# Kernel optimization log

Measured on AMD Instinct MI355X. Metric: run time of the kernel, lower is better.

The kernel has to match this reference:

```python
import jax, jax.numpy as jnp
import numpy as np

N = 100000   # nodes
E = 3200000  # edges
IN = 5
H = 128
L = 6
EPS = 1e-5

def _bn(x, g, b):
    # BatchNorm1d in training mode: batch stats over node dim, biased variance
    m = jnp.mean(x, axis=0)
    v = jnp.mean((x - m) ** 2, axis=0)
    return (x - m) * jax.lax.rsqrt(v + EPS) * g + b

def setup_inputs() -> dict:
    key = jax.random.key(0)
    ks = jax.random.split(key, 20)
    x = jax.random.normal(ks[0], (N, IN), dtype=jnp.float32)
    edge_index = jax.random.randint(ks[1], (2, E), 0, N, dtype=jnp.int64)
    batch = jnp.zeros((N,), dtype=jnp.int64)
    s = 0.05
    return {
        "x": x, "edge_index": edge_index, "batch": batch,
        "in_W": jax.random.normal(ks[2], (IN, H), jnp.float32) * s,
        "in_b": jnp.zeros((H,), jnp.float32),
        "in_g": jnp.ones((H,), jnp.float32),
        "in_beta": jnp.zeros((H,), jnp.float32),
        "conv_W": jax.random.normal(ks[3], (L, H, H), jnp.float32) * s,
        "conv_b": jnp.zeros((L, H), jnp.float32),
        "bn_g": jnp.ones((L, H), jnp.float32),
        "bn_beta": jnp.zeros((L, H), jnp.float32),
        "pW1": jax.random.normal(ks[4], (H, 32), jnp.float32) * s,
        "pb1": jnp.zeros((32,), jnp.float32),
        "pW2": jax.random.normal(ks[5], (32, 1), jnp.float32) * s,
        "pb2": jnp.zeros((1,), jnp.float32),
        "vW1": jax.random.normal(ks[6], (H, 64), jnp.float32) * s,
        "vb1": jnp.zeros((64,), jnp.float32),
        "vW2": jax.random.normal(ks[7], (64, 1), jnp.float32) * s,
        "vb2": jnp.zeros((1,), jnp.float32),
    }

def reference(x, edge_index, batch, in_W, in_b, in_g, in_beta,
              conv_W, conv_b, bn_g, bn_beta,
              pW1, pb1, pW2, pb2, vW1, vb1, vW2, vb2):
    n = x.shape[0]
    # GCN normalization with self-loops (computed once; depends only on edge_index)
    loops = jnp.arange(n, dtype=edge_index.dtype)
    src = jnp.concatenate([edge_index[0], loops])
    dst = jnp.concatenate([edge_index[1], loops])
    deg = jax.ops.segment_sum(jnp.ones_like(dst, dtype=x.dtype), dst, num_segments=n)
    dinv = jnp.where(deg > 0, jax.lax.rsqrt(deg), 0.0)
    norm = dinv[src] * dinv[dst]  # [E+N]

    def gcn(h, W, b):
        h = h @ W
        msg = h[src] * norm[:, None]
        return jax.ops.segment_sum(msg, dst, num_segments=n) + b

    h = jax.nn.relu(_bn(x @ in_W + in_b, in_g, in_beta))
    for i in range(L):
        h = jax.nn.relu(_bn(gcn(h, conv_W[i], conv_b[i]), bn_g[i], bn_beta[i])) + h

    policy_logits = (jax.nn.relu(h @ pW1 + pb1) @ pW2 + pb2)[:, 0]  # [N]

    # global_mean_pool over batch ids (single graph here, num_segments=1)
    num_graphs = 1
    sums = jax.ops.segment_sum(h, batch, num_segments=num_graphs)
    cnts = jax.ops.segment_sum(jnp.ones((n,), h.dtype), batch, num_segments=num_graphs)
    g = sums / jnp.maximum(cnts, 1.0)[:, None]  # [1, H]
    value = jnp.tanh(jax.nn.relu(g @ vW1 + vb1) @ vW2 + vb2)[:, 0]  # [1]
    return policy_logits, value
```

## Files before the change

### kernel.cpp

```cpp
#include <hip/hip_runtime.h>
#include <hip/hip_bf16.h>

typedef __hip_bfloat16 bf16;
typedef long long i64;
typedef unsigned short u16;
typedef __attribute__((ext_vector_type(8))) short bf16x8;
typedef __attribute__((ext_vector_type(4))) float f32x4;

#define EPSV 1e-5f
#define WINLEN 2560
#define CHUNK 64

static __device__ __forceinline__ float ldf(const void* p, size_t i, int fb) {
  return fb ? __bfloat162float(((const bf16*)p)[i]) : ((const float*)p)[i];
}
static __device__ __forceinline__ u16 f2b(float f) {
  unsigned int u = __float_as_uint(f);
  u += 0x7FFF + ((u >> 16) & 1);
  return (u16)(u >> 16);
}
static __device__ __forceinline__ float rb2f(u16 u) {
  return __uint_as_float(((unsigned int)u) << 16);
}
static __device__ __forceinline__ unsigned pk2(float a, float b) {
  return (unsigned)f2b(a) | ((unsigned)f2b(b) << 16);
}
static __device__ __forceinline__ float lo2f(unsigned w) { return __uint_as_float(w << 16); }
static __device__ __forceinline__ float hi2f(unsigned w) { return __uint_as_float(w & 0xFFFF0000u); }


__global__ void setup_kernel(const int* __restrict__ ei_w, const unsigned int* __restrict__ g,
                             int* __restrict__ eflag, int* __restrict__ fflag,
                             int* __restrict__ degcnt, int* __restrict__ fill,
                             int* __restrict__ wctr, int n) {
  int i = blockIdx.x * 256 + threadIdx.x;
  if (i < n) { degcnt[i] = 0; fill[i] = 0; }
  if (blockIdx.x == 0) {
    __shared__ int nz;
    if (threadIdx.x == 0) nz = 0;
    if (threadIdx.x < 32) wctr[threadIdx.x] = 0;
    __syncthreads();
    for (int k = threadIdx.x; k < 1024; k += 256)
      if (ei_w[2 * k + 1] != 0) atomicAdd(&nz, 1);
    __syncthreads();
    if (threadIdx.x == 0) {
      *eflag = (nz == 0) ? 1 : 0;
      *fflag = (g[0] == 0x3F803F80u) ? 1 : 0;
    }
  }
}


__global__ void __launch_bounds__(256) pre_merged_kernel(
    const void* __restrict__ x, const void* __restrict__ W, const void* __restrict__ b,
    const void* __restrict__ ei, const void* __restrict__ convW,
    const int* __restrict__ eflag, const int* __restrict__ fflag,
    int* __restrict__ degcnt, u16* __restrict__ pre, float* __restrict__ pi,
    u16* __restrict__ wf, int n, int in_dim, int e, int wtotal, int gi, int gf) {
  __shared__ float4 SS[256], QQ[256];
  int fb = *fflag;
  if ((int)blockIdx.x < gi) {
    int q = threadIdx.x & 31, g8 = threadIdx.x >> 5;
    int c = q * 4;
    float b0 = ldf(b, c, fb), b1 = ldf(b, c + 1, fb), b2v = ldf(b, c + 2, fb), b3 = ldf(b, c + 3, fb);
    float s0 = 0, s1 = 0, s2 = 0, s3 = 0, q0 = 0, q1 = 0, q2 = 0, q3 = 0;
    for (int node = blockIdx.x * 8 + g8; node < n; node += gi * 8) {
      float a0 = b0, a1 = b1, a2 = b2v, a3 = b3;
      for (int k = 0; k < in_dim; ++k) {
        float xv = ldf(x, (size_t)node * in_dim + k, fb);
        size_t w0 = (size_t)k * 128 + c;
        a0 = fmaf(xv, ldf(W, w0, fb), a0);
        a1 = fmaf(xv, ldf(W, w0 + 1, fb), a1);
        a2 = fmaf(xv, ldf(W, w0 + 2, fb), a2);
        a3 = fmaf(xv, ldf(W, w0 + 3, fb), a3);
      }
      unsigned w0p = pk2(a0, a1), w1p = pk2(a2, a3);
      *(uint2*)(pre + (size_t)node * 128 + c) = make_uint2(w0p, w1p);
      float r0 = lo2f(w0p), r1 = hi2f(w0p), r2 = lo2f(w1p), r3 = hi2f(w1p);
      s0 += r0; s1 += r1; s2 += r2; s3 += r3;
      q0 = fmaf(r0, r0, q0); q1 = fmaf(r1, r1, q1); q2 = fmaf(r2, r2, q2); q3 = fmaf(r3, r3, q3);
    }
    SS[threadIdx.x] = make_float4(s0, s1, s2, s3);
    QQ[threadIdx.x] = make_float4(q0, q1, q2, q3);
    __syncthreads();
    if (threadIdx.x < 32) {
      float4 a = SS[threadIdx.x], qq = QQ[threadIdx.x];
      for (int g = 1; g < 8; ++g) {
        float4 u = SS[g * 32 + threadIdx.x], w = QQ[g * 32 + threadIdx.x];
        a.x += u.x; a.y += u.y; a.z += u.z; a.w += u.w;
        qq.x += w.x; qq.y += w.y; qq.z += w.z; qq.w += w.w;
      }
      int cc = threadIdx.x * 4;
      *(float4*)(pi + (size_t)blockIdx.x * 256 + cc) = a;
      *(float4*)(pi + (size_t)blockIdx.x * 256 + 128 + cc) = qq;
    }
  } else if ((int)blockIdx.x < gi + gf) {
    int bid = blockIdx.x - gi;
    int k = bid & 7;
    int lo = (int)(((long long)n * k) >> 3);
    int hi = (int)(((long long)n * (k + 1)) >> 3);
    int stride = (gf >> 3) * 256;
    int fb64 = *eflag;
    for (int i = (bid >> 3) * 256 + threadIdx.x; i < e; i += stride) {
      int d;
      if (fb64) d = (int)((const i64*)ei)[(size_t)e + i];
      else      d = ((const int*)ei)[(size_t)e + i];
      if (d >= lo && d < hi) atomicAdd(&degcnt[d], 1);
    }
  } else {
    int bid = blockIdx.x - gi - gf;
    int i = bid * 256 + threadIdx.x;
    if (i < wtotal) {
      int l = i >> 14, r = i & 16383;
      int k = r >> 7, nn = r & 127;
      int s = k >> 5, quad = (k >> 3) & 3, j = k & 7;
      int ct = nn >> 4, n16 = nn & 15;
      wf[(size_t)l * 16384 + (ct * 4 + s) * 512 + quad * 128 + n16 * 8 + j] = f2b(ldf(convW, i, fb));
    }
  }
}


__global__ void __launch_bounds__(256) scanA_kernel(const int* __restrict__ deg,
                                                    int* __restrict__ rp,
                                                    int* __restrict__ bsum,
                                                    float* __restrict__ dinv, int n) {
  int base = blockIdx.x * 1024 + threadIdx.x * 4;
  int v0 = (base     < n) ? deg[base]     : 0;
  int v1 = (base + 1 < n) ? deg[base + 1] : 0;
  int v2 = (base + 2 < n) ? deg[base + 2] : 0;
  int v3 = (base + 3 < n) ? deg[base + 3] : 0;
  if (base     < n) dinv[base]     = rsqrtf((float)v0 + 1.0f);
  if (base + 1 < n) dinv[base + 1] = rsqrtf((float)v1 + 1.0f);
  if (base + 2 < n) dinv[base + 2] = rsqrtf((float)v2 + 1.0f);
  if (base + 3 < n) dinv[base + 3] = rsqrtf((float)v3 + 1.0f);
  int ts = v0 + v1 + v2 + v3;
  __shared__ int ls[256];
  ls[threadIdx.x] = ts;
  __syncthreads();
  for (int off = 1; off < 256; off <<= 1) {
    int u = (threadIdx.x >= off) ? ls[threadIdx.x - off] : 0;
    __syncthreads();
    ls[threadIdx.x] += u;
    __syncthreads();
  }
  int run = ls[threadIdx.x] - ts;
  if (base     < n) rp[base]     = run; run += v0;
  if (base + 1 < n) rp[base + 1] = run; run += v1;
  if (base + 2 < n) rp[base + 2] = run; run += v2;
  if (base + 3 < n) rp[base + 3] = run;
  if (threadIdx.x == 255) bsum[blockIdx.x] = ls[255];
}

__global__ void __launch_bounds__(256) scanB_kernel(int* __restrict__ bsum, int* __restrict__ rp,
                                                    int nb, int n, int e) {
  __shared__ int ls[256];
  int t = threadIdx.x;
  int v = (t < nb) ? bsum[t] : 0;
  ls[t] = v;
  __syncthreads();
  for (int off = 1; off < 256; off <<= 1) {
    int u = (t >= off) ? ls[t - off] : 0;
    __syncthreads();
    ls[t] += u;
    __syncthreads();
  }
  if (t < nb) bsum[t] = ls[t] - v;
  if (t == 0) rp[n] = e;
}

__global__ void scanC_kernel(int* __restrict__ rp, const int* __restrict__ bsum, int n) {
  int i = blockIdx.x * 256 + threadIdx.x;
  if (i < n) rp[i] += bsum[i >> 10];
}

__global__ void fill_kernel(const void* __restrict__ ei, const int* __restrict__ flag,
                            const int* __restrict__ row_ptr,
                            int* __restrict__ fill, int* __restrict__ csr_src, int e, int n) {
  int k = blockIdx.x & 7;
  int lo = (int)(((long long)n * k) >> 3);
  int hi = (int)(((long long)n * (k + 1)) >> 3);
  int stride = (gridDim.x >> 3) * 256;
  int fb64 = *flag;
  for (int i = (blockIdx.x >> 3) * 256 + threadIdx.x; i < e; i += stride) {
    int d;
    if (fb64) d = (int)((const i64*)ei)[(size_t)e + i];
    else      d = ((const int*)ei)[(size_t)e + i];
    if (d < lo || d >= hi) continue;
    int s;
    if (fb64) s = (int)((const i64*)ei)[i];
    else      s = ((const int*)ei)[i];
    int pos = row_ptr[d] + atomicAdd(&fill[d], 1);
    csr_src[pos] = s;
  }
}

__global__ void __launch_bounds__(1024) finalize_inproj_kernel(
    const float* __restrict__ pi, int nb,
    const void* __restrict__ g, const void* __restrict__ beta,
    const int* __restrict__ fflag,
    float* __restrict__ scale, float* __restrict__ shift,
    float inv_n) {
  __shared__ float RS[8][128], RQ[8][128];
  int fb = *fflag;
  int c = threadIdx.x & 127, r = threadIdx.x >> 7;
  float s = 0.f, s2 = 0.f;
#pragma unroll 4
  for (int b = r; b < nb; b += 8) {
    s  += pi[(size_t)b * 256 + c];
    s2 += pi[(size_t)b * 256 + 128 + c];
  }
  RS[r][c] = s; RQ[r][c] = s2;
  __syncthreads();
  if (threadIdx.x < 128) {
    float ts = 0.f, tq = 0.f;
#pragma unroll
    for (int i = 0; i < 8; ++i) { ts += RS[i][c]; tq += RQ[i][c]; }
    float mean = ts * inv_n;
    float var = tq * inv_n - mean * mean;
    float sc = ldf(g, c, fb) * rsqrtf(var + EPSV);
    scale[c] = sc;
    shift[c] = ldf(beta, c, fb) - mean * sc;
  }
}


__global__ void __launch_bounds__(256) gemm_bn_kernel(
    const u16* __restrict__ pre, u16* __restrict__ hbuf,
    const float* __restrict__ scale, const float* __restrict__ shift,
    const u16* __restrict__ wfL, const float* __restrict__ dinv,
    u16* __restrict__ u, int n, int use_res) {
  __shared__ u16 At[4][2048];
  int lane = threadIdx.x & 63;
  int wave = threadIdx.x >> 6;
  int n16 = lane & 15, quad = lane >> 4;
  u16* at = At[wave];
  int node = lane & 15;
  int cgrp = lane >> 4;
  int ntiles = (n + 15) >> 4;
  for (int tile = blockIdx.x * 4 + wave; tile < ntiles; tile += gridDim.x * 4) {
    int n0 = tile * 16;
    int gn = n0 + node;
#pragma unroll
    for (int r = 0; r < 8; ++r) {
      int c4 = r * 4 + cgrp;
      int c = c4 * 4;
      float4 h4 = make_float4(0.f, 0.f, 0.f, 0.f);
      if (gn < n) {
        uint2 pv = *(const uint2*)(pre + (size_t)gn * 128 + c);
        float4 sc = *(const float4*)(scale + c);
        float4 sh = *(const float4*)(shift + c);
        h4.x = fmaxf(fmaf(lo2f(pv.x), sc.x, sh.x), 0.f);
        h4.y = fmaxf(fmaf(hi2f(pv.x), sc.y, sh.y), 0.f);
        h4.z = fmaxf(fmaf(lo2f(pv.y), sc.z, sh.z), 0.f);
        h4.w = fmaxf(fmaf(hi2f(pv.y), sc.w, sh.w), 0.f);
        if (use_res) {
          uint2 rv = *(const uint2*)(hbuf + (size_t)gn * 128 + c);
          h4.x += lo2f(rv.x); h4.y += hi2f(rv.x);
          h4.z += lo2f(rv.y); h4.w += hi2f(rv.y);
        }
        *(uint2*)(hbuf + (size_t)gn * 128 + c) = make_uint2(pk2(h4.x, h4.y), pk2(h4.z, h4.w));
      }
      ushort4 uu;
      uu.x = f2b(h4.x); uu.y = f2b(h4.y); uu.z = f2b(h4.z); uu.w = f2b(h4.w);
      int s = c4 >> 3, qd = (c4 >> 1) & 3, j0 = (c4 & 1) * 4;
      *(ushort4*)(at + s * 512 + qd * 128 + node * 8 + j0) = uu;
    }
    __builtin_amdgcn_s_waitcnt(0);
    f32x4 acc[8];
#pragma unroll
    for (int ct = 0; ct < 8; ++ct) acc[ct] = (f32x4){0.f, 0.f, 0.f, 0.f};
#pragma unroll
    for (int s = 0; s < 4; ++s) {
      bf16x8 af = *(const bf16x8*)(at + s * 512 + lane * 8);
#pragma unroll
      for (int ct = 0; ct < 8; ++ct) {
        bf16x8 bfr = *(const bf16x8*)(wfL + (size_t)(ct * 4 + s) * 512 + lane * 8);
        acc[ct] = __builtin_amdgcn_mfma_f32_16x16x32_bf16(af, bfr, acc[ct], 0, 0, 0);
      }
    }
    float dv[4];
#pragma unroll
    for (int r = 0; r < 4; ++r) {
      int row = n0 + quad * 4 + r;
      dv[r] = (row < n) ? dinv[row] : 0.f;
    }
#pragma unroll
    for (int ct = 0; ct < 8; ++ct) {
#pragma unroll
      for (int r = 0; r < 4; ++r) {
        int row = n0 + quad * 4 + r;
        if (row < n)
          u[((size_t)(ct >> 1) * n + row) * 32 + (ct & 1) * 16 + n16] = f2b(acc[ct][r] * dv[r]);
      }
    }
  }
}


__global__ void __launch_bounds__(256) gather_stats_kernel(
    const int* __restrict__ row_ptr, const int* __restrict__ csr_src,
    const u16* __restrict__ u, const float* __restrict__ dinv,
    const void* __restrict__ b, const int* __restrict__ fflag,
    u16* __restrict__ pre, float* __restrict__ pg,
    int* __restrict__ wctr, int n, int nch, size_t bOff) {
  __shared__ int sm[WINLEN];
  __shared__ float SW[4][4][8], QW[4][4][8];
  __shared__ int curchunk;
  int fb = *fflag;
  int ct2 = blockIdx.x & 3;
  const u16* us = u + (size_t)ct2 * n * 32;
  int q = threadIdx.x & 3;
  int g = threadIdx.x >> 2;
  int c = ct2 * 32 + q * 8;
  float bias[8];
#pragma unroll
  for (int i = 0; i < 8; ++i) bias[i] = ldf(b, bOff + c + i, fb);
  float sA[8], qA[8];
#pragma unroll
  for (int i = 0; i < 8; ++i) { sA[i] = 0.f; qA[i] = 0.f; }

  for (;;) {
    __syncthreads();
    if (threadIdx.x == 0) curchunk = atomicAdd(&wctr[ct2], 1);
    __syncthreads();
    int ch = curchunk;
    if (ch >= nch) break;
    int c0 = ch * CHUNK;
    int node = c0 + g;
    int valid = node < n;
    int beg = valid ? row_ptr[node] : 0;
    int end = valid ? row_ptr[node + 1] : 0;
    int cend = c0 + CHUNK; if (cend > n) cend = n;
    int chunk_lo = row_ptr[c0];
    int chunk_hi = row_ptr[cend];
    float acc[8];
    if (valid) {
      uint4 su = *(const uint4*)(us + (size_t)node * 32 + q * 8);
      acc[0] = lo2f(su.x); acc[1] = hi2f(su.x);
      acc[2] = lo2f(su.y); acc[3] = hi2f(su.y);
      acc[4] = lo2f(su.z); acc[5] = hi2f(su.z);
      acc[6] = lo2f(su.w); acc[7] = hi2f(su.w);
    } else {
#pragma unroll
      for (int i = 0; i < 8; ++i) acc[i] = 0.f;
    }
    for (int wlo = chunk_lo; wlo < chunk_hi; wlo += WINLEN) {
      int wlen = chunk_hi - wlo; if (wlen > WINLEN) wlen = WINLEN;
      __syncthreads();
      for (int i = threadIdx.x; i < wlen; i += 256)
        sm[i] = __builtin_nontemporal_load(csr_src + wlo + i);
      __syncthreads();
      int j0 = beg > wlo ? beg : wlo;
      int j1 = end < wlo + wlen ? end : wlo + wlen;
      int j = j0;
#define ACC(UU) \
      acc[0] += lo2f(UU.x); acc[1] += hi2f(UU.x); \
      acc[2] += lo2f(UU.y); acc[3] += hi2f(UU.y); \
      acc[4] += lo2f(UU.z); acc[5] += hi2f(UU.z); \
      acc[6] += lo2f(UU.w); acc[7] += hi2f(UU.w);
      for (; j + 8 <= j1; j += 8) {
        int i0 = sm[j - wlo],     i1 = sm[j - wlo + 1], i2 = sm[j - wlo + 2], i3 = sm[j - wlo + 3];
        int i4 = sm[j - wlo + 4], i5 = sm[j - wlo + 5], i6 = sm[j - wlo + 6], i7 = sm[j - wlo + 7];
        uint4 U0 = *(const uint4*)(us + (size_t)i0 * 32 + q * 8);
        uint4 U1 = *(const uint4*)(us + (size_t)i1 * 32 + q * 8);
        uint4 U2 = *(const uint4*)(us + (size_t)i2 * 32 + q * 8);
        uint4 U3 = *(const uint4*)(us + (size_t)i3 * 32 + q * 8);
        uint4 U4 = *(const uint4*)(us + (size_t)i4 * 32 + q * 8);
        uint4 U5 = *(const uint4*)(us + (size_t)i5 * 32 + q * 8);
        uint4 U6 = *(const uint4*)(us + (size_t)i6 * 32 + q * 8);
        uint4 U7 = *(const uint4*)(us + (size_t)i7 * 32 + q * 8);
        ACC(U0) ACC(U1) ACC(U2) ACC(U3) ACC(U4) ACC(U5) ACC(U6) ACC(U7)
      }
      for (; j + 4 <= j1; j += 4) {
        int i0 = sm[j - wlo], i1 = sm[j - wlo + 1], i2 = sm[j - wlo + 2], i3 = sm[j - wlo + 3];
        uint4 U0 = *(const uint4*)(us + (size_t)i0 * 32 + q * 8);
        uint4 U1 = *(const uint4*)(us + (size_t)i1 * 32 + q * 8);
        uint4 U2 = *(const uint4*)(us + (size_t)i2 * 32 + q * 8);
        uint4 U3 = *(const uint4*)(us + (size_t)i3 * 32 + q * 8);
        ACC(U0) ACC(U1) ACC(U2) ACC(U3)
      }
      for (; j < j1; ++j) {
        int i0 = sm[j - wlo];
        uint4 U0 = *(const uint4*)(us + (size_t)i0 * 32 + q * 8);
        ACC(U0)
      }
#undef ACC
    }
    if (valid) {
      float dv = dinv[node];
      float o0 = fmaf(acc[0], dv, bias[0]), o1 = fmaf(acc[1], dv, bias[1]);
      float o2 = fmaf(acc[2], dv, bias[2]), o3 = fmaf(acc[3], dv, bias[3]);
      float o4 = fmaf(acc[4], dv, bias[4]), o5 = fmaf(acc[5], dv, bias[5]);
      float o6 = fmaf(acc[6], dv, bias[6]), o7 = fmaf(acc[7], dv, bias[7]);
      unsigned w0 = pk2(o0, o1), w1 = pk2(o2, o3), w2 = pk2(o4, o5), w3 = pk2(o6, o7);
      *(uint4*)(pre + (size_t)node * 128 + c) = make_uint4(w0, w1, w2, w3);
      float r0 = lo2f(w0), r1 = hi2f(w0), r2 = lo2f(w1), r3 = hi2f(w1);
      float r4 = lo2f(w2), r5 = hi2f(w2), r6 = lo2f(w3), r7 = hi2f(w3);
      sA[0] += r0; sA[1] += r1; sA[2] += r2; sA[3] += r3;
      sA[4] += r4; sA[5] += r5; sA[6] += r6; sA[7] += r7;
      qA[0] = fmaf(r0, r0, qA[0]); qA[1] = fmaf(r1, r1, qA[1]);
      qA[2] = fmaf(r2, r2, qA[2]); qA[3] = fmaf(r3, r3, qA[3]);
      qA[4] = fmaf(r4, r4, qA[4]); qA[5] = fmaf(r5, r5, qA[5]);
      qA[6] = fmaf(r6, r6, qA[6]); qA[7] = fmaf(r7, r7, qA[7]);
    }
  }
#pragma unroll
  for (int m = 4; m <= 32; m <<= 1) {
#pragma unroll
    for (int i = 0; i < 8; ++i) {
      sA[i] += __shfl_xor(sA[i], m, 64);
      qA[i] += __shfl_xor(qA[i], m, 64);
    }
  }
  int lane = threadIdx.x & 63, wv = threadIdx.x >> 6;
  if (lane < 4) {
#pragma unroll
    for (int i = 0; i < 8; ++i) { SW[wv][lane][i] = sA[i]; QW[wv][lane][i] = qA[i]; }
  }
  __syncthreads();
  if (threadIdx.x < 32) {
    int qq = threadIdx.x >> 3, i = threadIdx.x & 7;
    float a = SW[0][qq][i] + SW[1][qq][i] + SW[2][qq][i] + SW[3][qq][i];
    float b2 = QW[0][qq][i] + QW[1][qq][i] + QW[2][qq][i] + QW[3][qq][i];
    pg[(size_t)blockIdx.x * 64 + qq * 8 + i] = a;
    pg[(size_t)blockIdx.x * 64 + 32 + qq * 8 + i] = b2;
  }
}

__global__ void __launch_bounds__(1024) finalize_gather_kernel(
    const float* __restrict__ pg, int nbG,
    const void* __restrict__ g, const void* __restrict__ beta,
    const int* __restrict__ fflag,
    float* __restrict__ scale, float* __restrict__ shift,
    float inv_n, size_t off) {
  __shared__ float RS[8][128], RQ[8][128];
  int fb = *fflag;
  int c = threadIdx.x & 127, r = threadIdx.x >> 7;
  int ct2 = c >> 5, ic = c & 31;
  float s = 0.f, s2 = 0.f;
#pragma unroll 4
  for (int b = ct2 + 4 * r; b < nbG; b += 32) {
    s  += pg[(size_t)b * 64 + ic];
    s2 += pg[(size_t)b * 64 + 32 + ic];
  }
  RS[r][c] = s; RQ[r][c] = s2;
  __syncthreads();
  if (threadIdx.x < 128) {
    float ts = 0.f, tq = 0.f;
#pragma unroll
    for (int i = 0; i < 8; ++i) { ts += RS[i][c]; tq += RQ[i][c]; }
    float mean = ts * inv_n;
    float var = tq * inv_n - mean * mean;
    float sc = ldf(g, off + c, fb) * rsqrtf(var + EPSV);
    scale[c] = sc;
    shift[c] = ldf(beta, off + c, fb) - mean * sc;
  }
}


__global__ void __launch_bounds__(256) policy_pool_kernel(
    const u16* __restrict__ pre, const u16* __restrict__ hbuf,
    const float* __restrict__ scale, const float* __restrict__ shift,
    const void* __restrict__ pW1, const void* __restrict__ pb1,
    const void* __restrict__ pW2, const void* __restrict__ pb2,
    const int* __restrict__ fflag, float* __restrict__ pp,
    void* __restrict__ out, int n) {
  __shared__ float W1[128 * 32];
  __shared__ float B1v[32], W2v[32];
  int fb = *fflag;
  for (int i = threadIdx.x; i < 128 * 32; i += 256) W1[i] = ldf(pW1, i, fb);
  if (threadIdx.x < 32) {
    B1v[threadIdx.x] = ldf(pb1, threadIdx.x, fb);
    W2v[threadIdx.x] = ldf(pW2, threadIdx.x, fb);
  }
  __syncthreads();
  float bias2 = ldf(pb2, 0, fb);
  int q = threadIdx.x & 31, g8 = threadIdx.x >> 5;
  int c = q * 4;
  float4 sc = *(const float4*)(scale + c);
  float4 sh = *(const float4*)(shift + c);
  float cs0 = 0, cs1 = 0, cs2 = 0, cs3 = 0;
  for (int node = blockIdx.x * 8 + g8; node < n; node += gridDim.x * 8) {
    uint2 pv = *(const uint2*)(pre + (size_t)node * 128 + c);
    uint2 rv = *(const uint2*)(hbuf + (size_t)node * 128 + c);
    float4 h4;
    h4.x = fmaxf(fmaf(lo2f(pv.x), sc.x, sh.x), 0.f) + lo2f(rv.x);
    h4.y = fmaxf(fmaf(hi2f(pv.x), sc.y, sh.y), 0.f) + hi2f(rv.x);
    h4.z = fmaxf(fmaf(lo2f(pv.y), sc.z, sh.z), 0.f) + lo2f(rv.y);
    h4.w = fmaxf(fmaf(hi2f(pv.y), sc.w, sh.w), 0.f) + hi2f(rv.y);
    cs0 += h4.x; cs1 += h4.y; cs2 += h4.z; cs3 += h4.w;
    float acc = B1v[q];
#pragma unroll
    for (int k4 = 0; k4 < 32; ++k4) {
      float hx = __shfl(h4.x, k4, 32);
      float hy = __shfl(h4.y, k4, 32);
      float hz = __shfl(h4.z, k4, 32);
      float hw = __shfl(h4.w, k4, 32);
      int k = k4 * 4;
      acc = fmaf(hx, W1[k * 32 + q], acc);
      acc = fmaf(hy, W1[(k + 1) * 32 + q], acc);
      acc = fmaf(hz, W1[(k + 2) * 32 + q], acc);
      acc = fmaf(hw, W1[(k + 3) * 32 + q], acc);
    }
    acc = fmaxf(acc, 0.f) * W2v[q];
    for (int off = 16; off; off >>= 1) acc += __shfl_down(acc, off, 32);
    if (q == 0) {
      float v = acc + bias2;
      if (fb) ((bf16*)out)[node] = __float2bfloat16(v);
      else    ((float*)out)[node] = v;
    }
  }
  __shared__ float4 SS[256];
  SS[threadIdx.x] = make_float4(cs0, cs1, cs2, cs3);
  __syncthreads();
  if (threadIdx.x < 32) {
    float4 a = SS[threadIdx.x];
    for (int g = 1; g < 8; ++g) {
      float4 u = SS[g * 32 + threadIdx.x];
      a.x += u.x; a.y += u.y; a.z += u.z; a.w += u.w;
    }
    *(float4*)(pp + (size_t)blockIdx.x * 128 + threadIdx.x * 4) = a;
  }
}

__global__ void __launch_bounds__(1024) value_kernel(
    const float* __restrict__ pp, int nbP,
    const void* __restrict__ vW1, const void* __restrict__ vb1,
    const void* __restrict__ vW2, const void* __restrict__ vb2,
    const int* __restrict__ fflag,
    void* __restrict__ out, int n, float inv_n) {
  __shared__ float RS[8][128];
  __shared__ float gs[128];
  int fb = *fflag;
  int c = threadIdx.x & 127, r = threadIdx.x >> 7;
  float s = 0.f;
#pragma unroll 4
  for (int b = r; b < nbP; b += 8) s += pp[(size_t)b * 128 + c];
  RS[r][c] = s;
  __syncthreads();
  if (threadIdx.x < 128) {
    float t = 0.f;
#pragma unroll
    for (int i = 0; i < 8; ++i) t += RS[i][c];
    gs[c] = t;
  }
  __syncthreads();
  if (threadIdx.x < 64) {
    int cc = threadIdx.x;
    float acc = ldf(vb1, cc, fb);
    for (int k = 0; k < 128; ++k) acc = fmaf(gs[k] * inv_n, ldf(vW1, (size_t)k * 64 + cc, fb), acc);
    acc = fmaxf(acc, 0.f);
    float v = acc * ldf(vW2, cc, fb);
    for (int off = 32; off; off >>= 1) v += __shfl_down(v, off, 64);
    if (cc == 0) {
      float rr = tanhf(v + ldf(vb2, 0, fb));
      if (fb) ((bf16*)out)[n] = __float2bfloat16(rr);
      else    ((float*)out)[n] = rr;
    }
  }
}


extern "C" void kernel_launch(void* const* d_in, const int* in_sizes, int n_in,
                              void* d_out, int out_size, void* d_ws, size_t ws_size,
                              hipStream_t stream) {
  const void* x       = d_in[0];
  const void* ei      = d_in[1];
  const void* in_W    = d_in[3];
  const void* in_b    = d_in[4];
  const void* in_g    = d_in[5];
  const void* in_beta = d_in[6];
  const void* conv_W  = d_in[7];
  const void* conv_b  = d_in[8];
  const void* bn_g    = d_in[9];
  const void* bn_beta = d_in[10];
  const void* pW1     = d_in[11];
  const void* pb1     = d_in[12];
  const void* pW2     = d_in[13];
  const void* pb2     = d_in[14];
  const void* vW1     = d_in[15];
  const void* vb1     = d_in[16];
  const void* vW2     = d_in[17];
  const void* vb2     = d_in[18];

  const int H = 128;
  int in_dim = in_sizes[3] / H;
  int n      = in_sizes[0] / in_dim;
  int e      = in_sizes[1] / 2;
  int L      = in_sizes[7] / (H * H);

  const int GS  = 2048;
  const int GI  = 512;
  const int GP  = 1024;
  const int GF  = 2048;

  char* w = (char*)d_ws;
  u16*   u    = (u16*)w;   w += (size_t)n * H * sizeof(u16);
  u16*   pre  = (u16*)w;   w += (size_t)n * H * sizeof(u16);
  u16*   hbuf = (u16*)w;   w += (size_t)n * H * sizeof(u16);
  int*   csr_src  = (int*)w;   w += ((size_t)e + 16) * sizeof(int);
  int*   row_ptr  = (int*)w;   w += (size_t)(n + 1 + 15) / 16 * 16 * sizeof(int);
  int*   degcnt   = (int*)w;   w += (size_t)n * sizeof(int);
  int*   fillc    = (int*)w;   w += (size_t)n * sizeof(int);
  float* dinv     = (float*)w; w += (size_t)n * sizeof(float);
  float* scale = (float*)w; w += 128 * sizeof(float);
  float* shift = (float*)w; w += 128 * sizeof(float);
  int*   eflag = (int*)w;   w += 16 * sizeof(int);
  int*   fflag = (int*)w;   w += 16 * sizeof(int);
  int*   bsum  = (int*)w;   w += 256 * sizeof(int);
  int*   wctr  = (int*)w;   w += 32 * sizeof(int);
  u16*   wf    = (u16*)w;   w += (size_t)L * H * H * sizeof(u16);
  float* pi    = (float*)w; w += (size_t)GI * 256 * sizeof(float);
  float* pg    = (float*)w; w += (size_t)GS * 64 * sizeof(float);
  float* pp    = (float*)w; w += (size_t)GP * 128 * sizeof(float);

  int gN = (n + 255) / 256;
  int nb = (n + 1023) >> 10;
  int nch = (n + CHUNK - 1) / CHUNK;
  int wtotal = L * H * H;
  int GW = (wtotal + 255) / 256;
  float inv_n = 1.0f / (float)n;

  setup_kernel<<<gN, 256, 0, stream>>>((const int*)ei, (const unsigned int*)in_g,
                                       eflag, fflag, degcnt, fillc, wctr, n);
  pre_merged_kernel<<<GI + GF + GW, 256, 0, stream>>>(
      x, in_W, in_b, ei, conv_W, eflag, fflag, degcnt, pre, pi, wf,
      n, in_dim, e, wtotal, GI, GF);
  scanA_kernel<<<nb, 256, 0, stream>>>(degcnt, row_ptr, bsum, dinv, n);
  scanB_kernel<<<1, 256, 0, stream>>>(bsum, row_ptr, nb, n, e);
  scanC_kernel<<<gN, 256, 0, stream>>>(row_ptr, bsum, n);
  fill_kernel<<<GF, 256, 0, stream>>>(ei, eflag, row_ptr, fillc, csr_src, e, n);
  finalize_inproj_kernel<<<1, 1024, 0, stream>>>(pi, GI, in_g, in_beta, fflag, scale, shift, inv_n);

  for (int l = 0; l < L; ++l) {
    gemm_bn_kernel<<<2048, 256, 0, stream>>>(pre, hbuf, scale, shift, wf + (size_t)l * H * H,
                                             dinv, u, n, (l > 0) ? 1 : 0);
    gather_stats_kernel<<<GS, 256, 0, stream>>>(row_ptr, csr_src, u, dinv,
                                                conv_b, fflag, pre, pg, wctr + l * 4,
                                                n, nch, (size_t)l * H);
    finalize_gather_kernel<<<1, 1024, 0, stream>>>(pg, GS, bn_g, bn_beta, fflag, scale, shift,
                                                   inv_n, (size_t)l * H);
  }

  policy_pool_kernel<<<GP, 256, 0, stream>>>(pre, hbuf, scale, shift, pW1, pb1, pW2, pb2,
                                             fflag, pp, d_out, n);
  value_kernel<<<1, 1024, 0, stream>>>(pp, GP, vW1, vb1, vW2, vb2, fflag, d_out, n, inv_n);
}
```

Baseline: 1.721 ms.

## Partition CSR by source-node bucket so gathers stay within a cache-sized source range

Builds a bucketed CSR: edges are counted and placed per (source bucket, destination) slot, with 8 buckets chosen by shifting the source id. The scan now runs over 8n entries with a multi-pass block-sum scan, and the degree/dinv computation moves into scanC by summing the per-bucket counts. The gather kernel loops over buckets so that at any moment the blocks read u rows from one source range, which is meant to improve L2/MALL locality of the random row reads. In exchange it adds 8x more row-pointer reads and scan work, more window loop overhead per chunk, and larger count arrays.

```diff
diff --git a/kernel.cpp b/kernel.cpp
--- a/kernel.cpp
+++ b/kernel.cpp
@@ -10,6 +10,7 @@
 #define EPSV 1e-5f
 #define WINLEN 2560
 #define CHUNK 64
+#define NBUK 8
 
 static __device__ __forceinline__ float ldf(const void* p, size_t i, int fb) {
   return fb ? __bfloat162float(((const bf16*)p)[i]) : ((const float*)p)[i];
@@ -31,10 +32,10 @@
 
 __global__ void setup_kernel(const int* __restrict__ ei_w, const unsigned int* __restrict__ g,
                              int* __restrict__ eflag, int* __restrict__ fflag,
-                             int* __restrict__ degcnt, int* __restrict__ fill,
-                             int* __restrict__ wctr, int n) {
+                             int* __restrict__ deg2, int* __restrict__ fill2,
+                             int* __restrict__ wctr, int m8) {
   int i = blockIdx.x * 256 + threadIdx.x;
-  if (i < n) { degcnt[i] = 0; fill[i] = 0; }
+  if (i < m8) { deg2[i] = 0; fill2[i] = 0; }
   if (blockIdx.x == 0) {
     __shared__ int nz;
     if (threadIdx.x == 0) nz = 0;
@@ -55,8 +56,8 @@
     const void* __restrict__ x, const void* __restrict__ W, const void* __restrict__ b,
     const void* __restrict__ ei, const void* __restrict__ convW,
     const int* __restrict__ eflag, const int* __restrict__ fflag,
-    int* __restrict__ degcnt, u16* __restrict__ pre, float* __restrict__ pi,
-    u16* __restrict__ wf, int n, int in_dim, int e, int wtotal, int gi, int gf) {
+    int* __restrict__ deg2, u16* __restrict__ pre, float* __restrict__ pi,
+    u16* __restrict__ wf, int n, int in_dim, int e, int wtotal, int gi, int gf, int shift) {
   __shared__ float4 SS[256], QQ[256];
   int fb = *fflag;
   if ((int)blockIdx.x < gi) {
@@ -105,7 +106,13 @@
       int d;
       if (fb64) d = (int)((const i64*)ei)[(size_t)e + i];
       else      d = ((const int*)ei)[(size_t)e + i];
-      if (d >= lo && d < hi) atomicAdd(&degcnt[d], 1);
+      if (d >= lo && d < hi) {
+        int s;
+        if (fb64) s = (int)((const i64*)ei)[i];
+        else      s = ((const int*)ei)[i];
+        int bk = s >> shift;
+        atomicAdd(&deg2[(size_t)bk * n + d], 1);
+      }
     }
   } else {
     int bid = blockIdx.x - gi - gf;
@@ -123,17 +130,12 @@
 
 __global__ void __launch_bounds__(256) scanA_kernel(const int* __restrict__ deg,
                                                     int* __restrict__ rp,
-                                                    int* __restrict__ bsum,
-                                                    float* __restrict__ dinv, int n) {
+                                                    int* __restrict__ bsum, int m) {
   int base = blockIdx.x * 1024 + threadIdx.x * 4;
-  int v0 = (base     < n) ? deg[base]     : 0;
-  int v1 = (base + 1 < n) ? deg[base + 1] : 0;
-  int v2 = (base + 2 < n) ? deg[base + 2] : 0;
-  int v3 = (base + 3 < n) ? deg[base + 3] : 0;
-  if (base     < n) dinv[base]     = rsqrtf((float)v0 + 1.0f);
-  if (base + 1 < n) dinv[base + 1] = rsqrtf((float)v1 + 1.0f);
-  if (base + 2 < n) dinv[base + 2] = rsqrtf((float)v2 + 1.0f);
-  if (base + 3 < n) dinv[base + 3] = rsqrtf((float)v3 + 1.0f);
+  int v0 = (base     < m) ? deg[base]     : 0;
+  int v1 = (base + 1 < m) ? deg[base + 1] : 0;
+  int v2 = (base + 2 < m) ? deg[base + 2] : 0;
+  int v3 = (base + 3 < m) ? deg[base + 3] : 0;
   int ts = v0 + v1 + v2 + v3;
   __shared__ int ls[256];
   ls[threadIdx.x] = ts;
@@ -145,38 +147,57 @@
     __syncthreads();
   }
   int run = ls[threadIdx.x] - ts;
-  if (base     < n) rp[base]     = run; run += v0;
-  if (base + 1 < n) rp[base + 1] = run; run += v1;
-  if (base + 2 < n) rp[base + 2] = run; run += v2;
-  if (base + 3 < n) rp[base + 3] = run;
+  if (base     < m) rp[base]     = run; run += v0;
+  if (base + 1 < m) rp[base + 1] = run; run += v1;
+  if (base + 2 < m) rp[base + 2] = run; run += v2;
+  if (base + 3 < m) rp[base + 3] = run;
   if (threadIdx.x == 255) bsum[blockIdx.x] = ls[255];
 }
 
 __global__ void __launch_bounds__(256) scanB_kernel(int* __restrict__ bsum, int* __restrict__ rp,
-                                                    int nb, int n, int e) {
+                                                    int nb, int m, int e) {
   __shared__ int ls[256];
+  __shared__ int carry;
   int t = threadIdx.x;
-  int v = (t < nb) ? bsum[t] : 0;
-  ls[t] = v;
-  __syncthreads();
-  for (int off = 1; off < 256; off <<= 1) {
-    int u = (t >= off) ? ls[t - off] : 0;
-    __syncthreads();
-    ls[t] += u;
-    __syncthreads();
-  }
-  if (t < nb) bsum[t] = ls[t] - v;
-  if (t == 0) rp[n] = e;
-}
-
-__global__ void scanC_kernel(int* __restrict__ rp, const int* __restrict__ bsum, int n) {
+  if (t == 0) carry = 0;
+  __syncthreads();
+  for (int base = 0; base < nb; base += 256) {
+    int v = (base + t < nb) ? bsum[base + t] : 0;
+    ls[t] = v;
+    __syncthreads();
+    for (int off = 1; off < 256; off <<= 1) {
+      int u = (t >= off) ? ls[t - off] : 0;
+      __syncthreads();
+      ls[t] += u;
+      __syncthreads();
+    }
+    int ex = ls[t] - v + carry;
+    if (base + t < nb) bsum[base + t] = ex;
+    int tot = ls[255];
+    __syncthreads();
+    if (t == 0) carry += tot;
+    __syncthreads();
+  }
+  if (t == 0) rp[m] = e;
+}
+
+__global__ void scanC_kernel(int* __restrict__ rp, const int* __restrict__ bsum,
+                             const int* __restrict__ deg2, float* __restrict__ dinv,
+                             int n, int m) {
   int i = blockIdx.x * 256 + threadIdx.x;
-  if (i < n) rp[i] += bsum[i >> 10];
+  if (i < m) rp[i] += bsum[i >> 10];
+  if (i < n) {
+    int t = 0;
+#pragma unroll
+    for (int b = 0; b < NBUK; ++b) t += deg2[(size_t)b * n + i];
+    dinv[i] = rsqrtf((float)t + 1.0f);
+  }
 }
 
 __global__ void fill_kernel(const void* __restrict__ ei, const int* __restrict__ flag,
-                            const int* __restrict__ row_ptr,
-                            int* __restrict__ fill, int* __restrict__ csr_src, int e, int n) {
+                            const int* __restrict__ rp2,
+                            int* __restrict__ fill2, int* __restrict__ csr_src,
+                            int e, int n, int shift) {
   int k = blockIdx.x & 7;
   int lo = (int)(((long long)n * k) >> 3);
   int hi = (int)(((long long)n * (k + 1)) >> 3);
@@ -190,8 +211,10 @@
     int s;
     if (fb64) s = (int)((const i64*)ei)[i];
     else      s = ((const int*)ei)[i];
-    int pos = row_ptr[d] + atomicAdd(&fill[d], 1);
-    csr_src[pos] = s;
+    int bk = s >> shift;
+    size_t slot = (size_t)bk * n + d;
+    int pos = rp2[slot] + atomicAdd(&fill2[slot], 1);
+    __builtin_nontemporal_store(s, &csr_src[pos]);
   }
 }
 
@@ -299,7 +322,7 @@
 
 
 __global__ void __launch_bounds__(256) gather_stats_kernel(
-    const int* __restrict__ row_ptr, const int* __restrict__ csr_src,
+    const int* __restrict__ rp2, const int* __restrict__ csr_src,
     const u16* __restrict__ u, const float* __restrict__ dinv,
     const void* __restrict__ b, const int* __restrict__ fflag,
     u16* __restrict__ pre, float* __restrict__ pg,
@@ -329,11 +352,7 @@
     int c0 = ch * CHUNK;
     int node = c0 + g;
     int valid = node < n;
-    int beg = valid ? row_ptr[node] : 0;
-    int end = valid ? row_ptr[node + 1] : 0;
     int cend = c0 + CHUNK; if (cend > n) cend = n;
-    int chunk_lo = row_ptr[c0];
-    int chunk_hi = row_ptr[cend];
     float acc[8];
     if (valid) {
       uint4 su = *(const uint4*)(us + (size_t)node * 32 + q * 8);
@@ -345,47 +364,54 @@
 #pragma unroll
       for (int i = 0; i < 8; ++i) acc[i] = 0.f;
     }
-    for (int wlo = chunk_lo; wlo < chunk_hi; wlo += WINLEN) {
-      int wlen = chunk_hi - wlo; if (wlen > WINLEN) wlen = WINLEN;
-      __syncthreads();
-      for (int i = threadIdx.x; i < wlen; i += 256)
-        sm[i] = __builtin_nontemporal_load(csr_src + wlo + i);
-      __syncthreads();
-      int j0 = beg > wlo ? beg : wlo;
-      int j1 = end < wlo + wlen ? end : wlo + wlen;
-      int j = j0;
+    for (int bk = 0; bk < NBUK; ++bk) {
+      const int* rpb = rp2 + (size_t)bk * n;
+      int beg = valid ? rpb[node] : 0;
+      int end = valid ? rpb[node + 1] : 0;
+      int chunk_lo = rpb[c0];
+      int chunk_hi = rpb[cend];
+      for (int wlo = chunk_lo; wlo < chunk_hi; wlo += WINLEN) {
+        int wlen = chunk_hi - wlo; if (wlen > WINLEN) wlen = WINLEN;
+        __syncthreads();
+        for (int i = threadIdx.x; i < wlen; i += 256)
+          sm[i] = __builtin_nontemporal_load(csr_src + wlo + i);
+        __syncthreads();
+        int j0 = beg > wlo ? beg : wlo;
+        int j1 = end < wlo + wlen ? end : wlo + wlen;
+        int j = j0;
 #define ACC(UU) \
-      acc[0] += lo2f(UU.x); acc[1] += hi2f(UU.x); \
-      acc[2] += lo2f(UU.y); acc[3] += hi2f(UU.y); \
-      acc[4] += lo2f(UU.z); acc[5] += hi2f(UU.z); \
-      acc[6] += lo2f(UU.w); acc[7] += hi2f(UU.w);
-      for (; j + 8 <= j1; j += 8) {
-        int i0 = sm[j - wlo],     i1 = sm[j - wlo + 1], i2 = sm[j - wlo + 2], i3 = sm[j - wlo + 3];
-        int i4 = sm[j - wlo + 4], i5 = sm[j - wlo + 5], i6 = sm[j - wlo + 6], i7 = sm[j - wlo + 7];
-        uint4 U0 = *(const uint4*)(us + (size_t)i0 * 32 + q * 8);
-        uint4 U1 = *(const uint4*)(us + (size_t)i1 * 32 + q * 8);
-        uint4 U2 = *(const uint4*)(us + (size_t)i2 * 32 + q * 8);
-        uint4 U3 = *(const uint4*)(us + (size_t)i3 * 32 + q * 8);
-        uint4 U4 = *(const uint4*)(us + (size_t)i4 * 32 + q * 8);
-        uint4 U5 = *(const uint4*)(us + (size_t)i5 * 32 + q * 8);
-        uint4 U6 = *(const uint4*)(us + (size_t)i6 * 32 + q * 8);
-        uint4 U7 = *(const uint4*)(us + (size_t)i7 * 32 + q * 8);
-        ACC(U0) ACC(U1) ACC(U2) ACC(U3) ACC(U4) ACC(U5) ACC(U6) ACC(U7)
+        acc[0] += lo2f(UU.x); acc[1] += hi2f(UU.x); \
+        acc[2] += lo2f(UU.y); acc[3] += hi2f(UU.y); \
+        acc[4] += lo2f(UU.z); acc[5] += hi2f(UU.z); \
+        acc[6] += lo2f(UU.w); acc[7] += hi2f(UU.w);
+        for (; j + 8 <= j1; j += 8) {
+          int i0 = sm[j - wlo],     i1 = sm[j - wlo + 1], i2 = sm[j - wlo + 2], i3 = sm[j - wlo + 3];
+          int i4 = sm[j - wlo + 4], i5 = sm[j - wlo + 5], i6 = sm[j - wlo + 6], i7 = sm[j - wlo + 7];
+          uint4 U0 = *(const uint4*)(us + (size_t)i0 * 32 + q * 8);
+          uint4 U1 = *(const uint4*)(us + (size_t)i1 * 32 + q * 8);
+          uint4 U2 = *(const uint4*)(us + (size_t)i2 * 32 + q * 8);
+          uint4 U3 = *(const uint4*)(us + (size_t)i3 * 32 + q * 8);
+          uint4 U4 = *(const uint4*)(us + (size_t)i4 * 32 + q * 8);
+          uint4 U5 = *(const uint4*)(us + (size_t)i5 * 32 + q * 8);
+          uint4 U6 = *(const uint4*)(us + (size_t)i6 * 32 + q * 8);
+          uint4 U7 = *(const uint4*)(us + (size_t)i7 * 32 + q * 8);
+          ACC(U0) ACC(U1) ACC(U2) ACC(U3) ACC(U4) ACC(U5) ACC(U6) ACC(U7)
+        }
+        for (; j + 4 <= j1; j += 4) {
+          int i0 = sm[j - wlo], i1 = sm[j - wlo + 1], i2 = sm[j - wlo + 2], i3 = sm[j - wlo + 3];
+          uint4 U0 = *(const uint4*)(us + (size_t)i0 * 32 + q * 8);
+          uint4 U1 = *(const uint4*)(us + (size_t)i1 * 32 + q * 8);
+          uint4 U2 = *(const uint4*)(us + (size_t)i2 * 32 + q * 8);
+          uint4 U3 = *(const uint4*)(us + (size_t)i3 * 32 + q * 8);
+          ACC(U0) ACC(U1) ACC(U2) ACC(U3)
+        }
+        for (; j < j1; ++j) {
+          int i0 = sm[j - wlo];
+          uint4 U0 = *(const uint4*)(us + (size_t)i0 * 32 + q * 8);
+          ACC(U0)
+        }
+#undef ACC
       }
-      for (; j + 4 <= j1; j += 4) {
-        int i0 = sm[j - wlo], i1 = sm[j - wlo + 1], i2 = sm[j - wlo + 2], i3 = sm[j - wlo + 3];
-        uint4 U0 = *(const uint4*)(us + (size_t)i0 * 32 + q * 8);
-        uint4 U1 = *(const uint4*)(us + (size_t)i1 * 32 + q * 8);
-        uint4 U2 = *(const uint4*)(us + (size_t)i2 * 32 + q * 8);
-        uint4 U3 = *(const uint4*)(us + (size_t)i3 * 32 + q * 8);
-        ACC(U0) ACC(U1) ACC(U2) ACC(U3)
-      }
-      for (; j < j1; ++j) {
-        int i0 = sm[j - wlo];
-        uint4 U0 = *(const uint4*)(us + (size_t)i0 * 32 + q * 8);
-        ACC(U0)
-      }
-#undef ACC
     }
     if (valid) {
       float dv = dinv[node];
@@ -595,48 +621,53 @@
   const int GP  = 1024;
   const int GF  = 2048;
 
+  int m8 = NBUK * n;
+
   char* w = (char*)d_ws;
   u16*   u    = (u16*)w;   w += (size_t)n * H * sizeof(u16);
   u16*   pre  = (u16*)w;   w += (size_t)n * H * sizeof(u16);
   u16*   hbuf = (u16*)w;   w += (size_t)n * H * sizeof(u16);
   int*   csr_src  = (int*)w;   w += ((size_t)e + 16) * sizeof(int);
-  int*   row_ptr  = (int*)w;   w += (size_t)(n + 1 + 15) / 16 * 16 * sizeof(int);
-  int*   degcnt   = (int*)w;   w += (size_t)n * sizeof(int);
-  int*   fillc    = (int*)w;   w += (size_t)n * sizeof(int);
+  int*   rp2      = (int*)w;   w += (size_t)(m8 + 1 + 15) / 16 * 16 * sizeof(int);
+  int*   deg2     = (int*)w;   w += (size_t)m8 * sizeof(int);
+  int*   fill2    = (int*)w;   w += (size_t)m8 * sizeof(int);
   float* dinv     = (float*)w; w += (size_t)n * sizeof(float);
   float* scale = (float*)w; w += 128 * sizeof(float);
   float* shift = (float*)w; w += 128 * sizeof(float);
   int*   eflag = (int*)w;   w += 16 * sizeof(int);
   int*   fflag = (int*)w;   w += 16 * sizeof(int);
-  int*   bsum  = (int*)w;   w += 256 * sizeof(int);
+  int*   bsum  = (int*)w;   w += 1024 * sizeof(int);
   int*   wctr  = (int*)w;   w += 32 * sizeof(int);
   u16*   wf    = (u16*)w;   w += (size_t)L * H * H * sizeof(u16);
   float* pi    = (float*)w; w += (size_t)GI * 256 * sizeof(float);
   float* pg    = (float*)w; w += (size_t)GS * 64 * sizeof(float);
   float* pp    = (float*)w; w += (size_t)GP * 128 * sizeof(float);
 
-  int gN = (n + 255) / 256;
-  int nb = (n + 1023) >> 10;
+  int gS  = (m8 + 255) / 256;
+  int nbA = (m8 + 1023) >> 10;
+  int gC  = (m8 + 255) / 256;
   int nch = (n + CHUNK - 1) / CHUNK;
   int wtotal = L * H * H;
   int GW = (wtotal + 255) / 256;
   float inv_n = 1.0f / (float)n;
-
-  setup_kernel<<<gN, 256, 0, stream>>>((const int*)ei, (const unsigned int*)in_g,
-                                       eflag, fflag, degcnt, fillc, wctr, n);
+  int shiftB = 0;
+  while ((((long long)(n - 1)) >> shiftB) >= NBUK) shiftB++;
+
+  setup_kernel<<<gS, 256, 0, stream>>>((const int*)ei, (const unsigned int*)in_g,
+                                       eflag, fflag, deg2, fill2, wctr, m8);
   pre_merged_kernel<<<GI + GF + GW, 256, 0, stream>>>(
-      x, in_W, in_b, ei, conv_W, eflag, fflag, degcnt, pre, pi, wf,
-      n, in_dim, e, wtotal, GI, GF);
-  scanA_kernel<<<nb, 256, 0, stream>>>(degcnt, row_ptr, bsum, dinv, n);
-  scanB_kernel<<<1, 256, 0, stream>>>(bsum, row_ptr, nb, n, e);
-  scanC_kernel<<<gN, 256, 0, stream>>>(row_ptr, bsum, n);
-  fill_kernel<<<GF, 256, 0, stream>>>(ei, eflag, row_ptr, fillc, csr_src, e, n);
+      x, in_W, in_b, ei, conv_W, eflag, fflag, deg2, pre, pi, wf,
+      n, in_dim, e, wtotal, GI, GF, shiftB);
+  scanA_kernel<<<nbA, 256, 0, stream>>>(deg2, rp2, bsum, m8);
+  scanB_kernel<<<1, 256, 0, stream>>>(bsum, rp2, nbA, m8, e);
+  scanC_kernel<<<gC, 256, 0, stream>>>(rp2, bsum, deg2, dinv, n, m8);
+  fill_kernel<<<GF, 256, 0, stream>>>(ei, eflag, rp2, fill2, csr_src, e, n, shiftB);
   finalize_inproj_kernel<<<1, 1024, 0, stream>>>(pi, GI, in_g, in_beta, fflag, scale, shift, inv_n);
 
   for (int l = 0; l < L; ++l) {
     gemm_bn_kernel<<<2048, 256, 0, stream>>>(pre, hbuf, scale, shift, wf + (size_t)l * H * H,
                                              dinv, u, n, (l > 0) ? 1 : 0);
-    gather_stats_kernel<<<GS, 256, 0, stream>>>(row_ptr, csr_src, u, dinv,
+    gather_stats_kernel<<<GS, 256, 0, stream>>>(rp2, csr_src, u, dinv,
                                                 conv_b, fflag, pre, pg, wctr + l * 4,
                                                 n, nch, (size_t)l * H);
     finalize_gather_kernel<<<1, 1024, 0, stream>>>(pg, GS, bn_g, bn_beta, fflag, scale, shift,
```

Result: slower. 2.059 ms (+19.7%).
